# Performance work log

Hardware: AMD Instinct MI355X
Metric: run time of the kernel (lower is better)

The kernel has to match this reference:

```python
import jax, jax.numpy as jnp
import numpy as np

TOP_K = 2

def setup_inputs() -> dict:
    key = jax.random.key(0)
    k1, k2, k3, k4 = jax.random.split(key, 4)
    T, H, I, E = 8192, 2048, 4096, 8
    s = 0.02
    return {
        "hidden_states": jax.random.normal(k1, (T, H), dtype=jnp.float32),
        "router_w": jax.random.normal(k2, (E, H), dtype=jnp.float32) * s,
        "ws": jax.random.normal(k3, (E, 2 * I, H), dtype=jnp.float32) * s,  # [gate; up]
        "w2s": jax.random.normal(k4, (E, H, I), dtype=jnp.float32) * s,
    }

def reference(hidden_states, router_w, ws, w2s):
    # Router gating: softmax over experts, top-k, NO renormalization
    logits = hidden_states @ router_w.T              # [T, E]
    probs = jax.nn.softmax(logits, axis=-1)
    topv, topi = jax.lax.top_k(probs, TOP_K)         # [T, K]
    T, E = probs.shape
    I = w2s.shape[2]
    # Dense routing-weight matrix [T, E]; top_k indices are unique per token
    w = jnp.zeros_like(probs).at[jnp.arange(T)[:, None], topi].set(topv)
    out = jnp.zeros_like(hidden_states)
    for e in range(E):  # fixed small expert loop; avoids [T,E,2I] blowup
        gate = hidden_states @ ws[e, :I].T           # [T, I]
        up = hidden_states @ ws[e, I:].T             # [T, I]
        h = jax.nn.silu(gate) * up                   # SwiGLU
        out = out + w[:, e:e + 1] * (h @ w2s[e].T)   # combine
    return out
```

## Files before the change

kernel.cpp:

```cpp
#include <hip/hip_runtime.h>
#include <cstdint>
#include <cstddef>

#define T_TOK 8192
#define HDIM  2048
#define IDIM  4096
#define NEXP  8
#define MAXT  72

typedef __bf16 bf16x8 __attribute__((ext_vector_type(8)));
typedef float  f32x4  __attribute__((ext_vector_type(4)));

#define BARRIER() __builtin_amdgcn_s_barrier()
#define LGKM0()   do { asm volatile("s_waitcnt lgkmcnt(0)" ::: "memory"); __builtin_amdgcn_sched_barrier(0); } while (0)
#define VMW(n)    do { asm volatile("s_waitcnt vmcnt(" #n ")" ::: "memory"); } while (0)
#define PRIO1()   __builtin_amdgcn_s_setprio(1)
#define PRIO0()   __builtin_amdgcn_s_setprio(0)

__device__ __forceinline__ unsigned short f2bf(float f) {
    union { float f; unsigned u; } v; v.f = f;
    unsigned r = v.u + 0x7FFFu + ((v.u >> 16) & 1u);
    return (unsigned short)(r >> 16);
}

__device__ __forceinline__ void gload16(const void* g, void* l) {
    __builtin_amdgcn_global_load_lds((__attribute__((address_space(1))) void*)g,
                                     (__attribute__((address_space(3))) void*)l,
                                     16, 0, 0);
}

__global__ __launch_bounds__(256) void router_k(const float* __restrict__ hs,
                                                const float* __restrict__ rw,
                                                float* __restrict__ wgt,
                                                int* __restrict__ counts,
                                                int* __restrict__ lists,
                                                unsigned short* __restrict__ hs_bf) {
    int gid  = blockIdx.x * 256 + threadIdx.x;
    int tok  = gid >> 6;
    int lane = threadIdx.x & 63;
    const float* x = hs + (size_t)tok * HDIM;
    unsigned short* xb = hs_bf + (size_t)tok * HDIM;

    float acc[NEXP];
#pragma unroll
    for (int e = 0; e < NEXP; ++e) acc[e] = 0.f;
    for (int h = lane; h < HDIM; h += 64) {
        float xv = x[h];
        xb[h] = f2bf(xv);
#pragma unroll
        for (int e = 0; e < NEXP; ++e) acc[e] = fmaf(xv, rw[e * HDIM + h], acc[e]);
    }
#pragma unroll
    for (int off = 32; off > 0; off >>= 1) {
#pragma unroll
        for (int e = 0; e < NEXP; ++e) acc[e] += __shfl_xor(acc[e], off, 64);
    }
    if (lane == 0) {
        float m = acc[0];
#pragma unroll
        for (int e = 1; e < NEXP; ++e) m = fmaxf(m, acc[e]);
        float p[NEXP]; float s = 0.f;
#pragma unroll
        for (int e = 0; e < NEXP; ++e) { p[e] = expf(acc[e] - m); s += p[e]; }
        float inv = 1.f / s;
        int i1 = 0;
#pragma unroll
        for (int e = 1; e < NEXP; ++e) if (acc[e] > acc[i1]) i1 = e;
        int i2 = -1;
#pragma unroll
        for (int e = 0; e < NEXP; ++e) if (e != i1 && (i2 < 0 || acc[e] > acc[i2])) i2 = e;
#pragma unroll
        for (int e = 0; e < NEXP; ++e)
            wgt[(size_t)tok * NEXP + e] = (e == i1 || e == i2) ? p[e] * inv : 0.f;
        int p1 = atomicAdd(&counts[i1], 1);
        lists[i1 * T_TOK + p1] = tok;
        int p2 = atomicAdd(&counts[i2], 1);
        lists[i2 * T_TOK + p2] = (1 << 16) | tok;
    }
}

__global__ void plan_k(const int* __restrict__ counts, int* __restrict__ offs,
                       int* __restrict__ desc, int* __restrict__ ntiles) {
    if (threadIdx.x == 0 && blockIdx.x == 0) {
        int off = 0, n = 0;
        for (int e = 0; e < NEXP; ++e) {
            offs[e] = off;
            int nt = (counts[e] + 255) >> 8;
            for (int t = 0; t < nt; ++t) desc[n++] = (e << 16) | t;
            off += nt * 256;
        }
        *ntiles = n;
    }
}

__global__ __launch_bounds__(256) void cvt_k(const float* __restrict__ in,
                                             unsigned short* __restrict__ out, long n4) {
    long i      = (long)blockIdx.x * 256 + threadIdx.x;
    long stride = (long)gridDim.x * 256;
    const float4* in4 = (const float4*)in;
    ushort4* out4 = (ushort4*)out;
    for (long j = i; j < n4; j += stride) {
        float4 v = in4[j];
        ushort4 o;
        o.x = f2bf(v.x); o.y = f2bf(v.y); o.z = f2bf(v.z); o.w = f2bf(v.w);
        out4[j] = o;
    }
}

__global__ __launch_bounds__(512, 2) void gemm1_k(const unsigned short* __restrict__ A,
                                                  const unsigned short* __restrict__ Wall,
                                                  unsigned short* __restrict__ Hout,
                                                  const int* __restrict__ lists,
                                                  const int* __restrict__ counts,
                                                  const int* __restrict__ offs,
                                                  const int* __restrict__ desc,
                                                  const int* __restrict__ ntiles) {
    const int slot = blockIdx.y;
    if (slot >= *ntiles) return;
    const int dsc = desc[slot];
    const int e = dsc >> 16, tt = dsc & 0xFFFF;
    const int cnt = counts[e];
    const int t0 = tt * 256;
    const int* list = lists + e * T_TOK;
    const unsigned short* W = Wall + (size_t)e * 2 * IDIM * HDIM;
    const int hbase = offs[e];
    const int n0 = blockIdx.x * 128;

    extern __shared__ __align__(16) char lds[];

    const int tid  = threadIdx.x;
    const int lane = tid & 63;
    const int wid  = tid >> 6;
    const int wr   = wid >> 2;
    const int wc   = wid & 3;

    const int prow = tid >> 3;
    const int pcol = (tid & 7) * 16;
    const int lcol = (pcol ^ ((prow & 7) << 4)) >> 1;
    unsigned aoff[4];
#pragma unroll
    for (int i = 0; i < 4; ++i) {
        int g = t0 + i * 64 + prow;
        int tok = list[(g < cnt) ? g : t0] & 0xFFFF;
        aoff[i] = (unsigned)tok * HDIM + lcol;
    }
    unsigned goff[2], uoff[2];
#pragma unroll
    for (int i = 0; i < 2; ++i) {
        goff[i] = (unsigned)(n0 + i * 64 + prow) * HDIM + lcol;
        uoff[i] = (unsigned)(IDIM + n0 + i * 64 + prow) * HDIM + lcol;
    }
    const int dst = tid * 16;

#define SG_AH0(b, t) do { unsigned k0_ = (unsigned)((t) & 31) * 64;      \
    gload16(A + aoff[0] + k0_, lds + (b) * 32768 + dst);                 \
    gload16(A + aoff[1] + k0_, lds + (b) * 32768 + 8192 + dst); } while (0)
#define SG_AH1(b, t) do { unsigned k0_ = (unsigned)((t) & 31) * 64;      \
    gload16(A + aoff[2] + k0_, lds + (b) * 32768 + 16384 + dst);         \
    gload16(A + aoff[3] + k0_, lds + (b) * 32768 + 24576 + dst); } while (0)
#define SG_G(b, t) do { unsigned k0_ = (unsigned)((t) & 31) * 64;        \
    gload16(W + goff[0] + k0_, lds + 65536 + (b) * 16384 + dst);         \
    gload16(W + goff[1] + k0_, lds + 65536 + (b) * 16384 + 8192 + dst); } while (0)
#define SG_U(b, t) do { unsigned k0_ = (unsigned)((t) & 31) * 64;        \
    gload16(W + uoff[0] + k0_, lds + 98304 + (b) * 16384 + dst);         \
    gload16(W + uoff[1] + k0_, lds + 98304 + (b) * 16384 + 8192 + dst); } while (0)

    const int frd = (lane & 7) << 4;
    const int cb0 = (((lane >> 4) * 16)     ) ^ frd;
    const int cb1 = (((lane >> 4) * 16) | 64) ^ frd;
    const int arow = (wr * 64 + (lane & 15)) * 128;
    const int brow = (wc * 32 + (lane & 15)) * 128;

    f32x4 accg[8][2], accu[8][2];
#pragma unroll
    for (int mi = 0; mi < 8; ++mi)
#pragma unroll
        for (int ni = 0; ni < 2; ++ni) {
            accg[mi][ni] = (f32x4){0.f, 0.f, 0.f, 0.f};
            accu[mi][ni] = (f32x4){0.f, 0.f, 0.f, 0.f};
        }

    SG_AH0(0, 0); SG_G(0, 0); SG_U(0, 0); SG_AH1(0, 0);
    SG_AH0(1, 1); SG_G(1, 1);
    VMW(0);
    BARRIER();

    const int NT = HDIM / 64;
    for (int kt = 0; kt < NT; ++kt) {
        const int b  = kt & 1;
        const int bn = b ^ 1;
        const char* la = lds + b * 32768 + arow;
        const char* lg = lds + 65536 + b * 16384 + brow;
        const char* lu = lds + 98304 + b * 16384 + brow;
        bf16x8 a0[2][4], bg[2][2], bu[2][2];

#pragma unroll
        for (int mi = 0; mi < 4; ++mi) {
            a0[0][mi] = *(const bf16x8*)(la + mi * 2048 + cb0);
            a0[1][mi] = *(const bf16x8*)(la + mi * 2048 + cb1);
        }
#pragma unroll
        for (int ni = 0; ni < 2; ++ni) {
            bg[0][ni] = *(const bf16x8*)(lg + ni * 2048 + cb0);
            bg[1][ni] = *(const bf16x8*)(lg + ni * 2048 + cb1);
        }
        SG_AH1(bn, kt + 1);
        BARRIER(); LGKM0(); PRIO1();
#pragma unroll
        for (int ks = 0; ks < 2; ++ks)
#pragma unroll
            for (int mi = 0; mi < 4; ++mi)
#pragma unroll
                for (int ni = 0; ni < 2; ++ni)
                    accg[mi][ni] = __builtin_amdgcn_mfma_f32_16x16x32_bf16(a0[ks][mi], bg[ks][ni], accg[mi][ni], 0, 0, 0);
        PRIO0();
        VMW(6);
        BARRIER();

#pragma unroll
        for (int ni = 0; ni < 2; ++ni) {
            bu[0][ni] = *(const bf16x8*)(lu + ni * 2048 + cb0);
            bu[1][ni] = *(const bf16x8*)(lu + ni * 2048 + cb1);
        }
        SG_U(bn, kt + 1);
        BARRIER(); LGKM0(); PRIO1();
#pragma unroll
        for (int ks = 0; ks < 2; ++ks)
#pragma unroll
            for (int mi = 0; mi < 4; ++mi)
#pragma unroll
                for (int ni = 0; ni < 2; ++ni)
                    accu[mi][ni] = __builtin_amdgcn_mfma_f32_16x16x32_bf16(a0[ks][mi], bu[ks][ni], accu[mi][ni], 0, 0, 0);
        PRIO0(); BARRIER();

#pragma unroll
        for (int mi = 0; mi < 4; ++mi) {
            a0[0][mi] = *(const bf16x8*)(la + 16384 + mi * 2048 + cb0);
            a0[1][mi] = *(const bf16x8*)(la + 16384 + mi * 2048 + cb1);
        }
        SG_AH0(b, kt + 2);
        BARRIER(); LGKM0(); PRIO1();
#pragma unroll
        for (int ks = 0; ks < 2; ++ks)
#pragma unroll
            for (int mi = 0; mi < 4; ++mi)
#pragma unroll
                for (int ni = 0; ni < 2; ++ni)
                    accg[mi + 4][ni] = __builtin_amdgcn_mfma_f32_16x16x32_bf16(a0[ks][mi], bg[ks][ni], accg[mi + 4][ni], 0, 0, 0);
        PRIO0(); BARRIER();

        SG_G(b, kt + 2);
        PRIO1();
#pragma unroll
        for (int ks = 0; ks < 2; ++ks)
#pragma unroll
            for (int mi = 0; mi < 4; ++mi)
#pragma unroll
                for (int ni = 0; ni < 2; ++ni)
                    accu[mi + 4][ni] = __builtin_amdgcn_mfma_f32_16x16x32_bf16(a0[ks][mi], bu[ks][ni], accu[mi + 4][ni], 0, 0, 0);
        PRIO0();
        VMW(8);
        BARRIER();
    }
    VMW(0);
#undef SG_AH0
#undef SG_AH1
#undef SG_G
#undef SG_U

#pragma unroll
    for (int mi = 0; mi < 8; ++mi)
#pragma unroll
        for (int ni = 0; ni < 2; ++ni)
#pragma unroll
            for (int j = 0; j < 4; ++j) {
                int qr = mi >> 2, m = mi & 3;
                int row = hbase + t0 + qr * 128 + wr * 64 + m * 16 + ((lane >> 4) << 2) + j;
                int col = n0 + wc * 32 + ni * 16 + (lane & 15);
                float g = accg[mi][ni][j], u = accu[mi][ni][j];
                float hv = (g / (1.f + expf(-g))) * u;
                Hout[(size_t)row * IDIM + col] = f2bf(hv);
            }
}

__global__ __launch_bounds__(512, 2) void gemm2_k(const unsigned short* __restrict__ Ah,
                                                  const unsigned short* __restrict__ Ball,
                                                  const float* __restrict__ wgt,
                                                  float* __restrict__ outP,
                                                  const int* __restrict__ lists,
                                                  const int* __restrict__ counts,
                                                  const int* __restrict__ offs,
                                                  const int* __restrict__ desc,
                                                  const int* __restrict__ ntiles) {
    const int slot = blockIdx.y;
    if (slot >= *ntiles) return;
    const int dsc = desc[slot];
    const int e = dsc >> 16, tt = dsc & 0xFFFF;
    const int cnt = counts[e];
    const int t0 = tt * 256;
    const int* list = lists + e * T_TOK;
    const unsigned short* B = Ball + (size_t)e * HDIM * IDIM;
    const int hbase = offs[e];
    const int n0 = blockIdx.x * 256;

    extern __shared__ __align__(16) char lds[];

    const int tid  = threadIdx.x;
    const int lane = tid & 63;
    const int wid  = tid >> 6;
    const int wr   = wid >> 2;
    const int wc   = wid & 3;

    const int prow = tid >> 3;
    const int pcol = (tid & 7) * 16;
    const int lcol = (pcol ^ ((prow & 7) << 4)) >> 1;
    unsigned aoff[4], boff[4];
#pragma unroll
    for (int i = 0; i < 4; ++i) {
        aoff[i] = (unsigned)(hbase + t0 + i * 64 + prow) * IDIM + lcol;
        boff[i] = (unsigned)(n0 + i * 64 + prow) * IDIM + lcol;
    }
    const int dst = tid * 16;

#define SG_AH0(b, t) do { unsigned k0_ = (unsigned)((t) & 63) * 64;       \
    gload16(Ah + aoff[0] + k0_, lds + (b) * 32768 + dst);                 \
    gload16(Ah + aoff[1] + k0_, lds + (b) * 32768 + 8192 + dst); } while (0)
#define SG_AH1(b, t) do { unsigned k0_ = (unsigned)((t) & 63) * 64;       \
    gload16(Ah + aoff[2] + k0_, lds + (b) * 32768 + 16384 + dst);         \
    gload16(Ah + aoff[3] + k0_, lds + (b) * 32768 + 24576 + dst); } while (0)
#define SG_BH0(b, t) do { unsigned k0_ = (unsigned)((t) & 63) * 64;       \
    gload16(B + boff[0] + k0_, lds + 65536 + (b) * 32768 + dst);          \
    gload16(B + boff[1] + k0_, lds + 65536 + (b) * 32768 + 8192 + dst); } while (0)
#define SG_BH1(b, t) do { unsigned k0_ = (unsigned)((t) & 63) * 64;       \
    gload16(B + boff[2] + k0_, lds + 65536 + (b) * 32768 + 16384 + dst);  \
    gload16(B + boff[3] + k0_, lds + 65536 + (b) * 32768 + 24576 + dst); } while (0)

    const int frd = (lane & 7) << 4;
    const int cb0 = (((lane >> 4) * 16)     ) ^ frd;
    const int cb1 = (((lane >> 4) * 16) | 64) ^ frd;
    const int arow = (wr * 64 + (lane & 15)) * 128;
    const int brow = (wc * 64 + (lane & 15)) * 128;

    f32x4 acc[8][4];
#pragma unroll
    for (int mi = 0; mi < 8; ++mi)
#pragma unroll
        for (int ni = 0; ni < 4; ++ni) acc[mi][ni] = (f32x4){0.f, 0.f, 0.f, 0.f};

    SG_AH0(0, 0); SG_BH0(0, 0); SG_AH1(0, 0); SG_BH1(0, 0);
    SG_AH0(1, 1); SG_BH0(1, 1);
    VMW(0);
    BARRIER();

    const int NT = IDIM / 64;
    for (int kt = 0; kt < NT; ++kt) {
        const int b  = kt & 1;
        const int bn = b ^ 1;
        const char* la = lds + b * 32768 + arow;
        const char* lb = lds + 65536 + b * 32768 + brow;
        bf16x8 a0[2][4], bb[2][4];

#pragma unroll
        for (int mi = 0; mi < 4; ++mi) {
            a0[0][mi] = *(const bf16x8*)(la + mi * 2048 + cb0);
            a0[1][mi] = *(const bf16x8*)(la + mi * 2048 + cb1);
        }
#pragma unroll
        for (int ni = 0; ni < 2; ++ni) {
            bb[0][ni] = *(const bf16x8*)(lb + ni * 2048 + cb0);
            bb[1][ni] = *(const bf16x8*)(lb + ni * 2048 + cb1);
        }
        SG_AH1(bn, kt + 1);
        BARRIER(); LGKM0(); PRIO1();
#pragma unroll
        for (int ks = 0; ks < 2; ++ks)
#pragma unroll
            for (int mi = 0; mi < 4; ++mi)
#pragma unroll
                for (int ni = 0; ni < 2; ++ni)
                    acc[mi][ni] = __builtin_amdgcn_mfma_f32_16x16x32_bf16(a0[ks][mi], bb[ks][ni], acc[mi][ni], 0, 0, 0);
        PRIO0(); BARRIER();

#pragma unroll
        for (int ni = 0; ni < 2; ++ni) {
            bb[0][ni + 2] = *(const bf16x8*)(lb + (ni + 2) * 2048 + cb0);
            bb[1][ni + 2] = *(const bf16x8*)(lb + (ni + 2) * 2048 + cb1);
        }
        SG_BH1(bn, kt + 1);
        BARRIER(); LGKM0(); PRIO1();
#pragma unroll
        for (int ks = 0; ks < 2; ++ks)
#pragma unroll
            for (int mi = 0; mi < 4; ++mi)
#pragma unroll
                for (int ni = 0; ni < 2; ++ni)
                    acc[mi][ni + 2] = __builtin_amdgcn_mfma_f32_16x16x32_bf16(a0[ks][mi], bb[ks][ni + 2], acc[mi][ni + 2], 0, 0, 0);
        PRIO0(); BARRIER();

#pragma unroll
        for (int mi = 0; mi < 4; ++mi) {
            a0[0][mi] = *(const bf16x8*)(la + 16384 + mi * 2048 + cb0);
            a0[1][mi] = *(const bf16x8*)(la + 16384 + mi * 2048 + cb1);
        }
        SG_AH0(b, kt + 2);
        BARRIER(); LGKM0(); PRIO1();
#pragma unroll
        for (int ks = 0; ks < 2; ++ks)
#pragma unroll
            for (int mi = 0; mi < 4; ++mi)
#pragma unroll
                for (int ni = 0; ni < 2; ++ni)
                    acc[mi + 4][ni] = __builtin_amdgcn_mfma_f32_16x16x32_bf16(a0[ks][mi], bb[ks][ni], acc[mi + 4][ni], 0, 0, 0);
        PRIO0(); BARRIER();

        SG_BH0(b, kt + 2);
        PRIO1();
#pragma unroll
        for (int ks = 0; ks < 2; ++ks)
#pragma unroll
            for (int mi = 0; mi < 4; ++mi)
#pragma unroll
                for (int ni = 0; ni < 2; ++ni)
                    acc[mi + 4][ni + 2] = __builtin_amdgcn_mfma_f32_16x16x32_bf16(a0[ks][mi], bb[ks][ni + 2], acc[mi + 4][ni + 2], 0, 0, 0);
        PRIO0();
        VMW(4);
        BARRIER();
    }
    VMW(0);
#undef SG_AH0
#undef SG_AH1
#undef SG_BH0
#undef SG_BH1

#pragma unroll
    for (int mi = 0; mi < 8; ++mi) {
        int qr = mi >> 2, m = mi & 3;
#pragma unroll
        for (int j = 0; j < 4; ++j) {
            int g = t0 + qr * 128 + wr * 64 + m * 16 + ((lane >> 4) << 2) + j;
            if (g < cnt) {
                int ent = list[g];
                int tok = ent & 0xFFFF;
                int sl  = ent >> 16;
                float w = wgt[(size_t)tok * NEXP + e];
                float* o = outP + (size_t)sl * T_TOK * HDIM + (size_t)tok * HDIM;
#pragma unroll
                for (int ni = 0; ni < 4; ++ni) {
                    int col = n0 + wc * 64 + ni * 16 + (lane & 15);
                    o[col] = w * acc[mi][ni][j];
                }
            }
        }
    }
}

__global__ __launch_bounds__(256) void combine_k(const float* __restrict__ p0,
                                                 const float* __restrict__ p1,
                                                 float* __restrict__ out, long n4) {
    long i      = (long)blockIdx.x * 256 + threadIdx.x;
    long stride = (long)gridDim.x * 256;
    const float4* a4 = (const float4*)p0;
    const float4* b4 = (const float4*)p1;
    float4* o4 = (float4*)out;
    for (long j = i; j < n4; j += stride) {
        float4 a = a4[j], b = b4[j];
        o4[j] = make_float4(a.x + b.x, a.y + b.y, a.z + b.z, a.w + b.w);
    }
}

extern "C" void kernel_launch(void* const* d_in, const int* in_sizes, int n_in,
                              void* d_out, int out_size, void* d_ws, size_t ws_size,
                              hipStream_t stream) {
    const float* hs  = (const float*)d_in[0];
    const float* rw  = (const float*)d_in[1];
    const float* ws  = (const float*)d_in[2];
    const float* w2s = (const float*)d_in[3];
    float* out = (float*)d_out;

    char* wsp = (char*)d_ws;
    unsigned short* hs_bf = (unsigned short*)(wsp);
    unsigned short* w_bf  = (unsigned short*)(wsp + 33554432ULL);
    unsigned short* w2_bf = (unsigned short*)(wsp + 301989888ULL);
    unsigned short* h_bf  = (unsigned short*)(wsp + 436207616ULL);
    float*          outP  = (float*)(wsp + 587202560ULL);
    float*          wgt   = (float*)(wsp + 721420288ULL);
    int*            counts = (int*)(wsp + 721682432ULL);
    int*            offs   = (int*)(wsp + 721682560ULL);
    int*            lists  = (int*)(wsp + 721682688ULL);
    int*            desc   = (int*)(wsp + 721944832ULL);
    int*            ntiles = (int*)(wsp + 721945344ULL);

    hipMemsetAsync(counts, 0, NEXP * sizeof(int), stream);
    cvt_k<<<4096, 256, 0, stream>>>(ws, w_bf, (long)NEXP * 2 * IDIM * HDIM / 4);
    cvt_k<<<4096, 256, 0, stream>>>(w2s, w2_bf, (long)NEXP * HDIM * IDIM / 4);
    router_k<<<(T_TOK * 64) / 256, 256, 0, stream>>>(hs, rw, wgt, counts, lists, hs_bf);
    plan_k<<<1, 64, 0, stream>>>(counts, offs, desc, ntiles);

    gemm1_k<<<dim3(IDIM / 128, MAXT), 512, 131072, stream>>>(
        hs_bf, w_bf, h_bf, lists, counts, offs, desc, ntiles);
    gemm2_k<<<dim3(HDIM / 256, MAXT), 512, 131072, stream>>>(
        h_bf, w2_bf, wgt, outP, lists, counts, offs, desc, ntiles);
    combine_k<<<2048, 256, 0, stream>>>(outP, outP + (size_t)T_TOK * HDIM, out,
                                        (long)T_TOK * HDIM / 4);
}
```

Measured before the change: 1.373 ms.

## Halve gemm2 M tile to 128 rows and relax gemm1 vmcnt waits

gemm2 now processes 128-token tiles, selected by a new grid z dimension, instead of 256-token tiles. This halves the A staging buffers, shrinks LDS to 96KB and cuts the accumulators to 4x4, and blocks whose tile starts past the expert's count exit early, which trims wasted work on partial tiles. The price is that each B (w2) tile is loaded twice as often, so less data is reused per block. gemm1's vmcnt waits are loosened (drop the mid-iteration wait, use vmcnt 4 at the end and in the prologue) so more loads stay in flight, which risks reading stale LDS if the counts are wrong.

```diff
diff --git a/kernel.cpp b/kernel.cpp
--- a/kernel.cpp
+++ b/kernel.cpp
@@ -182,7 +182,7 @@
 
     SG_AH0(0, 0); SG_G(0, 0); SG_U(0, 0); SG_AH1(0, 0);
     SG_AH0(1, 1); SG_G(1, 1);
-    VMW(0);
+    VMW(4);
     BARRIER();
 
     const int NT = HDIM / 64;
@@ -213,9 +213,7 @@
 #pragma unroll
                 for (int ni = 0; ni < 2; ++ni)
                     accg[mi][ni] = __builtin_amdgcn_mfma_f32_16x16x32_bf16(a0[ks][mi], bg[ks][ni], accg[mi][ni], 0, 0, 0);
-        PRIO0();
-        VMW(6);
-        BARRIER();
+        PRIO0(); BARRIER();
 
 #pragma unroll
         for (int ni = 0; ni < 2; ++ni) {
@@ -259,7 +257,7 @@
                 for (int ni = 0; ni < 2; ++ni)
                     accu[mi + 4][ni] = __builtin_amdgcn_mfma_f32_16x16x32_bf16(a0[ks][mi], bu[ks][ni], accu[mi + 4][ni], 0, 0, 0);
         PRIO0();
-        VMW(8);
+        VMW(4);
         BARRIER();
     }
     VMW(0);
@@ -297,7 +295,8 @@
     const int dsc = desc[slot];
     const int e = dsc >> 16, tt = dsc & 0xFFFF;
     const int cnt = counts[e];
-    const int t0 = tt * 256;
+    const int t0 = tt * 256 + blockIdx.z * 128;
+    if (t0 >= cnt) return;
     const int* list = lists + e * T_TOK;
     const unsigned short* B = Ball + (size_t)e * HDIM * IDIM;
     const int hbase = offs[e];
@@ -314,26 +313,24 @@
     const int prow = tid >> 3;
     const int pcol = (tid & 7) * 16;
     const int lcol = (pcol ^ ((prow & 7) << 4)) >> 1;
-    unsigned aoff[4], boff[4];
-#pragma unroll
-    for (int i = 0; i < 4; ++i) {
+    unsigned aoff[2], boff[4];
+#pragma unroll
+    for (int i = 0; i < 2; ++i)
         aoff[i] = (unsigned)(hbase + t0 + i * 64 + prow) * IDIM + lcol;
+#pragma unroll
+    for (int i = 0; i < 4; ++i)
         boff[i] = (unsigned)(n0 + i * 64 + prow) * IDIM + lcol;
-    }
     const int dst = tid * 16;
 
-#define SG_AH0(b, t) do { unsigned k0_ = (unsigned)((t) & 63) * 64;       \
-    gload16(Ah + aoff[0] + k0_, lds + (b) * 32768 + dst);                 \
-    gload16(Ah + aoff[1] + k0_, lds + (b) * 32768 + 8192 + dst); } while (0)
-#define SG_AH1(b, t) do { unsigned k0_ = (unsigned)((t) & 63) * 64;       \
-    gload16(Ah + aoff[2] + k0_, lds + (b) * 32768 + 16384 + dst);         \
-    gload16(Ah + aoff[3] + k0_, lds + (b) * 32768 + 24576 + dst); } while (0)
+#define SG_A(b, t) do { unsigned k0_ = (unsigned)((t) & 63) * 64;         \
+    gload16(Ah + aoff[0] + k0_, lds + (b) * 16384 + dst);                 \
+    gload16(Ah + aoff[1] + k0_, lds + (b) * 16384 + 8192 + dst); } while (0)
 #define SG_BH0(b, t) do { unsigned k0_ = (unsigned)((t) & 63) * 64;       \
-    gload16(B + boff[0] + k0_, lds + 65536 + (b) * 32768 + dst);          \
-    gload16(B + boff[1] + k0_, lds + 65536 + (b) * 32768 + 8192 + dst); } while (0)
+    gload16(B + boff[0] + k0_, lds + 32768 + (b) * 32768 + dst);          \
+    gload16(B + boff[1] + k0_, lds + 32768 + (b) * 32768 + 8192 + dst); } while (0)
 #define SG_BH1(b, t) do { unsigned k0_ = (unsigned)((t) & 63) * 64;       \
-    gload16(B + boff[2] + k0_, lds + 65536 + (b) * 32768 + 16384 + dst);  \
-    gload16(B + boff[3] + k0_, lds + 65536 + (b) * 32768 + 24576 + dst); } while (0)
+    gload16(B + boff[2] + k0_, lds + 32768 + (b) * 32768 + 16384 + dst);  \
+    gload16(B + boff[3] + k0_, lds + 32768 + (b) * 32768 + 24576 + dst); } while (0)
 
     const int frd = (lane & 7) << 4;
     const int cb0 = (((lane >> 4) * 16)     ) ^ frd;
@@ -341,23 +338,23 @@
     const int arow = (wr * 64 + (lane & 15)) * 128;
     const int brow = (wc * 64 + (lane & 15)) * 128;
 
-    f32x4 acc[8][4];
-#pragma unroll
-    for (int mi = 0; mi < 8; ++mi)
+    f32x4 acc[4][4];
+#pragma unroll
+    for (int mi = 0; mi < 4; ++mi)
 #pragma unroll
         for (int ni = 0; ni < 4; ++ni) acc[mi][ni] = (f32x4){0.f, 0.f, 0.f, 0.f};
 
-    SG_AH0(0, 0); SG_BH0(0, 0); SG_AH1(0, 0); SG_BH1(0, 0);
-    SG_AH0(1, 1); SG_BH0(1, 1);
-    VMW(0);
+    SG_A(0, 0); SG_BH0(0, 0); SG_BH1(0, 0);
+    SG_A(1, 1); SG_BH0(1, 1);
+    VMW(4);
     BARRIER();
 
     const int NT = IDIM / 64;
     for (int kt = 0; kt < NT; ++kt) {
         const int b  = kt & 1;
         const int bn = b ^ 1;
-        const char* la = lds + b * 32768 + arow;
-        const char* lb = lds + 65536 + b * 32768 + brow;
+        const char* la = lds + b * 16384 + arow;
+        const char* lb = lds + 32768 + b * 32768 + brow;
         bf16x8 a0[2][4], bb[2][4];
 
 #pragma unroll
@@ -370,7 +367,7 @@
             bb[0][ni] = *(const bf16x8*)(lb + ni * 2048 + cb0);
             bb[1][ni] = *(const bf16x8*)(lb + ni * 2048 + cb1);
         }
-        SG_AH1(bn, kt + 1);
+        SG_BH1(bn, kt + 1);
         BARRIER(); LGKM0(); PRIO1();
 #pragma unroll
         for (int ks = 0; ks < 2; ++ks)
@@ -386,7 +383,8 @@
             bb[0][ni + 2] = *(const bf16x8*)(lb + (ni + 2) * 2048 + cb0);
             bb[1][ni + 2] = *(const bf16x8*)(lb + (ni + 2) * 2048 + cb1);
         }
-        SG_BH1(bn, kt + 1);
+        SG_A(b, kt + 2);
+        SG_BH0(b, kt + 2);
         BARRIER(); LGKM0(); PRIO1();
 #pragma unroll
         for (int ks = 0; ks < 2; ++ks)
@@ -395,49 +393,20 @@
 #pragma unroll
                 for (int ni = 0; ni < 2; ++ni)
                     acc[mi][ni + 2] = __builtin_amdgcn_mfma_f32_16x16x32_bf16(a0[ks][mi], bb[ks][ni + 2], acc[mi][ni + 2], 0, 0, 0);
-        PRIO0(); BARRIER();
-
-#pragma unroll
-        for (int mi = 0; mi < 4; ++mi) {
-            a0[0][mi] = *(const bf16x8*)(la + 16384 + mi * 2048 + cb0);
-            a0[1][mi] = *(const bf16x8*)(la + 16384 + mi * 2048 + cb1);
-        }
-        SG_AH0(b, kt + 2);
-        BARRIER(); LGKM0(); PRIO1();
-#pragma unroll
-        for (int ks = 0; ks < 2; ++ks)
-#pragma unroll
-            for (int mi = 0; mi < 4; ++mi)
-#pragma unroll
-                for (int ni = 0; ni < 2; ++ni)
-                    acc[mi + 4][ni] = __builtin_amdgcn_mfma_f32_16x16x32_bf16(a0[ks][mi], bb[ks][ni], acc[mi + 4][ni], 0, 0, 0);
-        PRIO0(); BARRIER();
-
-        SG_BH0(b, kt + 2);
-        PRIO1();
-#pragma unroll
-        for (int ks = 0; ks < 2; ++ks)
-#pragma unroll
-            for (int mi = 0; mi < 4; ++mi)
-#pragma unroll
-                for (int ni = 0; ni < 2; ++ni)
-                    acc[mi + 4][ni + 2] = __builtin_amdgcn_mfma_f32_16x16x32_bf16(a0[ks][mi], bb[ks][ni + 2], acc[mi + 4][ni + 2], 0, 0, 0);
         PRIO0();
         VMW(4);
         BARRIER();
     }
     VMW(0);
-#undef SG_AH0
-#undef SG_AH1
+#undef SG_A
 #undef SG_BH0
 #undef SG_BH1
 
 #pragma unroll
-    for (int mi = 0; mi < 8; ++mi) {
-        int qr = mi >> 2, m = mi & 3;
+    for (int mi = 0; mi < 4; ++mi) {
 #pragma unroll
         for (int j = 0; j < 4; ++j) {
-            int g = t0 + qr * 128 + wr * 64 + m * 16 + ((lane >> 4) << 2) + j;
+            int g = t0 + wr * 64 + mi * 16 + ((lane >> 4) << 2) + j;
             if (g < cnt) {
                 int ent = list[g];
                 int tok = ent & 0xFFFF;
@@ -498,7 +467,7 @@
 
     gemm1_k<<<dim3(IDIM / 128, MAXT), 512, 131072, stream>>>(
         hs_bf, w_bf, h_bf, lists, counts, offs, desc, ntiles);
-    gemm2_k<<<dim3(HDIM / 256, MAXT), 512, 131072, stream>>>(
+    gemm2_k<<<dim3(HDIM / 256, MAXT, 2), 512, 98304, stream>>>(
         h_bf, w2_bf, wgt, outP, lists, counts, offs, desc, ntiles);
     combine_k<<<2048, 256, 0, stream>>>(outP, outP + (size_t)T_TOK * HDIM, out,
                                         (long)T_TOK * HDIM / 4);
```

New measurement: 1.406 ms. 1.02x slower.
